# Optimization experiments

Measured on AMD Instinct MI355X. Metric: run time of the kernel, lower is better.

## Reference

```python
import jax, jax.numpy as jnp
import numpy as np

NEG_INF = -1e9  # matches masked_fill value -1000000000.0
SLOPE = 0.2     # LeakyReLU negative slope


def setup_inputs() -> dict:
    key = jax.random.key(0)
    k1, k2, k3, k4 = jax.random.split(key, 4)
    B, N, Fin, Fout = 16, 1024, 256, 256
    h = jax.random.normal(k1, (B, N, Fin), dtype=jnp.float32)
    adj = jax.random.randint(k2, (B, N, N), 0, 2, dtype=jnp.int32)
    W = jax.random.normal(k3, (Fin, Fout), dtype=jnp.float32) * (1.0 / np.sqrt(Fin))
    a = jax.random.normal(k4, (2 * Fout,), dtype=jnp.float32) * (1.0 / np.sqrt(2 * Fout))
    return {"h": h, "adj": adj, "W": W, "a": a}


def reference(h, adj, W, a):
    # h: [B,N,Fin], adj: [B,N,N] (0/1), W: [Fin,Fout], a: [2*Fout]
    Fout = W.shape[1]
    Wh = jnp.einsum("bnf,fo->bno", h, W)            # [B,N,Fout]
    a1, a2 = a[:Fout], a[Fout:]
    # e[b,i,j] = leakyrelu( Wh[b,i]·a1 + Wh[b,j]·a2 )  == a(cat(Wh_i, Wh_j))
    f1 = Wh @ a1                                     # [B,N]
    f2 = Wh @ a2                                     # [B,N]
    e = jax.nn.leaky_relu(f1[:, :, None] + f2[:, None, :], negative_slope=SLOPE)
    e = jnp.where(adj == 0, NEG_INF, e)              # mask non-edges
    attention = jax.nn.softmax(e, axis=-1)           # [B,N,N]
    # dropout is identity at eval / p=0
    h_prime = jnp.einsum("bij,bjo->bio", attention, Wh)  # [B,N,Fout]
    return h_prime
```

## Files before the change

### kernel.cpp

```cpp
#include <hip/hip_runtime.h>

typedef __attribute__((ext_vector_type(8))) short bf16x8;
typedef __attribute__((ext_vector_type(4))) float f32x4;

__device__ __forceinline__ unsigned short f2bf(float x) {
    unsigned int u = __float_as_uint(x);
    u += 0x7FFFu + ((u >> 16) & 1u);
    return (unsigned short)(u >> 16);
}

__device__ __forceinline__ void gl_lds16(const void* g, void* l) {
    __builtin_amdgcn_global_load_lds(
        (__attribute__((address_space(1))) void*)((void*)g),
        (__attribute__((address_space(3))) void*)l, 16, 0, 0);
}

__global__ __launch_bounds__(256) void prep(const float* __restrict__ W,
                                            short* __restrict__ WbT) {
    __shared__ float tile[32][33];
    const int t = threadIdx.x;
    const int bx = blockIdx.x & 7, by = blockIdx.x >> 3;
    const int r0 = by * 32, c0 = bx * 32;
    const int lr = t >> 5, lc = t & 31;
#pragma unroll
    for (int q = 0; q < 4; ++q)
        tile[q * 8 + lr][lc] = W[(r0 + q * 8 + lr) * 256 + c0 + lc];
    __syncthreads();
#pragma unroll
    for (int q = 0; q < 4; ++q)
        WbT[(c0 + q * 8 + lr) * 256 + r0 + lc] = (short)f2bf(tile[lc][q * 8 + lr]);
}

__global__ __launch_bounds__(256, 4) void wh_f12(const float* __restrict__ h,
                                                 const short* __restrict__ WbT,
                                                 const float* __restrict__ a,
                                                 short* __restrict__ WhT,
                                                 float* __restrict__ f1,
                                                 float* __restrict__ f2) {
    __shared__ short hA[16][264];
    __shared__ float sp[2][4][16];
    const int t = threadIdx.x;
    const int wid = t >> 6, lane = t & 63;
    const int quad = lane >> 4, l15 = lane & 15;
    const int m0 = blockIdx.x * 16;

    {
        const int r = t >> 4, c0 = (t & 15) * 16;
        const float* hp = h + (size_t)(m0 + r) * 256 + c0;
        float4 v0 = *(const float4*)(hp + 0), v1 = *(const float4*)(hp + 4);
        float4 v2 = *(const float4*)(hp + 8), v3 = *(const float4*)(hp + 12);
        bf16x8 w0, w1;
        w0[0] = (short)f2bf(v0.x); w0[1] = (short)f2bf(v0.y);
        w0[2] = (short)f2bf(v0.z); w0[3] = (short)f2bf(v0.w);
        w0[4] = (short)f2bf(v1.x); w0[5] = (short)f2bf(v1.y);
        w0[6] = (short)f2bf(v1.z); w0[7] = (short)f2bf(v1.w);
        w1[0] = (short)f2bf(v2.x); w1[1] = (short)f2bf(v2.y);
        w1[2] = (short)f2bf(v2.z); w1[3] = (short)f2bf(v2.w);
        w1[4] = (short)f2bf(v3.x); w1[5] = (short)f2bf(v3.y);
        w1[6] = (short)f2bf(v3.z); w1[7] = (short)f2bf(v3.w);
        *(bf16x8*)&hA[r][c0] = w0;
        *(bf16x8*)&hA[r][c0 + 8] = w1;
    }
    __syncthreads();

    f32x4 acc[4] = {};
#pragma unroll
    for (int kt = 0; kt < 8; ++kt) {
        const int k0 = kt * 32;
        bf16x8 av = *(const bf16x8*)&hA[l15][k0 + quad * 8];
#pragma unroll
        for (int ft = 0; ft < 4; ++ft) {
            const int f = wid * 64 + ft * 16 + l15;
            bf16x8 bv = *(const bf16x8*)(WbT + (size_t)f * 256 + k0 + quad * 8);
            acc[ft] = __builtin_amdgcn_mfma_f32_16x16x32_bf16(av, bv, acc[ft], 0, 0, 0);
        }
    }

    const int b = m0 >> 10;
    const int il0 = (m0 & 1023) + quad * 4;
#pragma unroll
    for (int ft = 0; ft < 4; ++ft) {
        const int f = wid * 64 + ft * 16 + l15;
        ushort4 pk;
        pk.x = f2bf(acc[ft][0]);
        pk.y = f2bf(acc[ft][1]);
        pk.z = f2bf(acc[ft][2]);
        pk.w = f2bf(acc[ft][3]);
        *(ushort4*)(WhT + ((size_t)b << 18) + (size_t)f * 1024 + il0) = pk;
    }

    float a1v[4], a2v[4];
#pragma unroll
    for (int ft = 0; ft < 4; ++ft) {
        a1v[ft] = a[wid * 64 + ft * 16 + l15];
        a2v[ft] = a[256 + wid * 64 + ft * 16 + l15];
    }
    float p1[4] = {}, p2[4] = {};
#pragma unroll
    for (int ft = 0; ft < 4; ++ft)
#pragma unroll
        for (int r = 0; r < 4; ++r) {
            p1[r] += acc[ft][r] * a1v[ft];
            p2[r] += acc[ft][r] * a2v[ft];
        }
#pragma unroll
    for (int off = 1; off < 16; off <<= 1)
#pragma unroll
        for (int r = 0; r < 4; ++r) {
            p1[r] += __shfl_xor(p1[r], off);
            p2[r] += __shfl_xor(p2[r], off);
        }
    if (l15 == 0)
#pragma unroll
        for (int r = 0; r < 4; ++r) {
            sp[0][wid][quad * 4 + r] = p1[r];
            sp[1][wid][quad * 4 + r] = p2[r];
        }
    __syncthreads();
    if (t < 16) {
        f1[m0 + t] = sp[0][0][t] + sp[0][1][t] + sp[0][2][t] + sp[0][3][t];
        f2[m0 + t] = sp[1][0][t] + sp[1][1][t] + sp[1][2][t] + sp[1][3][t];
    }
}

__global__ __launch_bounds__(256) void stats_p(const int* __restrict__ adj,
                                               const float* __restrict__ f1g,
                                               const float* __restrict__ f2g,
                                               short* __restrict__ P) {
    const int wid = threadIdx.x >> 6, lane = threadIdx.x & 63;
    const int gid = blockIdx.x * 4 + wid;
    const int b = gid >> 10;
    const int* arow = adj + (size_t)gid * 1024;
    const float* f2b = f2g + (b << 10);
    const float f1r = f1g[gid];

    float e[16];
#pragma unroll
    for (int c = 0; c < 4; ++c) {
        int4 av = *(const int4*)(arow + lane * 4 + c * 256);
        float4 fv = *(const float4*)(f2b + lane * 4 + c * 256);
        float x0 = f1r + fv.x, x1 = f1r + fv.y, x2 = f1r + fv.z, x3 = f1r + fv.w;
        e[c * 4 + 0] = av.x ? fmaxf(x0, 0.2f * x0) : -3.0e38f;
        e[c * 4 + 1] = av.y ? fmaxf(x1, 0.2f * x1) : -3.0e38f;
        e[c * 4 + 2] = av.z ? fmaxf(x2, 0.2f * x2) : -3.0e38f;
        e[c * 4 + 3] = av.w ? fmaxf(x3, 0.2f * x3) : -3.0e38f;
    }
    float m = e[0];
#pragma unroll
    for (int q = 1; q < 16; ++q) m = fmaxf(m, e[q]);
#pragma unroll
    for (int off = 32; off; off >>= 1) m = fmaxf(m, __shfl_xor(m, off));

    float p[16];
    float l = 0.f;
#pragma unroll
    for (int q = 0; q < 16; ++q) { p[q] = __expf(e[q] - m); l += p[q]; }
#pragma unroll
    for (int off = 32; off; off >>= 1) l += __shfl_xor(l, off);
    const float invl = 1.0f / l;

    short* prow = P + (size_t)gid * 1024;
#pragma unroll
    for (int c = 0; c < 4; ++c) {
        ushort4 pk;
        pk.x = f2bf(p[c * 4 + 0] * invl);
        pk.y = f2bf(p[c * 4 + 1] * invl);
        pk.z = f2bf(p[c * 4 + 2] * invl);
        pk.w = f2bf(p[c * 4 + 3] * invl);
        *(ushort4*)(prow + lane * 4 + c * 256) = pk;
    }
}

__global__ __launch_bounds__(256, 2) void agg(const short* __restrict__ P,
                                              const short* __restrict__ WhT,
                                              float* __restrict__ out) {
    __shared__ short As[128 * 32];
    __shared__ short Bs[64 * 32];

    const int t = threadIdx.x;
    const int wid = t >> 6, lane = t & 63;
    const int quad = lane >> 4, l15 = lane & 15;
    const int m0 = blockIdx.x * 128, n0 = blockIdx.y * 64, b = blockIdx.z;

    const short* Pb = P + ((size_t)b << 20);
    const short* Wb = WhT + ((size_t)b << 18);

    const int ar = t >> 2, aq = (t & 3) * 8;
    const short* ga0 = Pb + (size_t)(m0 + ar) * 1024 + aq;
    const short* ga1 = Pb + (size_t)(m0 + 64 + ar) * 1024 + aq;
    const short* gb0 = Wb + (size_t)(n0 + ar) * 1024 + aq;
    short* lA0 = As + t * 8;
    short* lA1 = As + 2048 + t * 8;
    short* lB0 = Bs + t * 8;

    f32x4 acc[2][4] = {};

    for (int k0 = 0; k0 < 1024; k0 += 32) {
        gl_lds16(ga0 + k0, lA0);
        gl_lds16(ga1 + k0, lA1);
        gl_lds16(gb0 + k0, lB0);
        __syncthreads();

        bf16x8 av[2], bv[4];
#pragma unroll
        for (int mf = 0; mf < 2; ++mf)
            av[mf] = *(const bf16x8*)(As + (wid * 32 + mf * 16 + l15) * 32 + quad * 8);
#pragma unroll
        for (int nf = 0; nf < 4; ++nf)
            bv[nf] = *(const bf16x8*)(Bs + (nf * 16 + l15) * 32 + quad * 8);
#pragma unroll
        for (int mf = 0; mf < 2; ++mf)
#pragma unroll
            for (int nf = 0; nf < 4; ++nf)
                acc[mf][nf] = __builtin_amdgcn_mfma_f32_16x16x32_bf16(av[mf], bv[nf], acc[mf][nf], 0, 0, 0);
        __syncthreads();
    }

#pragma unroll
    for (int mf = 0; mf < 2; ++mf) {
        const int i = m0 + wid * 32 + mf * 16 + quad * 4;
#pragma unroll
        for (int nf = 0; nf < 4; ++nf) {
            float* op = out + (size_t)((b << 10) + i) * 256 + n0 + nf * 16 + l15;
            op[0]   = acc[mf][nf][0];
            op[256] = acc[mf][nf][1];
            op[512] = acc[mf][nf][2];
            op[768] = acc[mf][nf][3];
        }
    }
}

extern "C" void kernel_launch(void* const* d_in, const int* in_sizes, int n_in,
                              void* d_out, int out_size, void* d_ws, size_t ws_size,
                              hipStream_t stream) {
    const float* h   = (const float*)d_in[0];
    const int*   adj = (const int*)d_in[1];
    const float* W   = (const float*)d_in[2];
    const float* a   = (const float*)d_in[3];
    float* out = (float*)d_out;

    short* WbT = (short*)d_ws;
    float* f1  = (float*)(WbT + 65536);
    float* f2  = f1 + 16384;
    short* WhT = (short*)(f2 + 16384);
    short* P   = WhT + 16 * 256 * 1024;

    prep<<<64, 256, 0, stream>>>(W, WbT);
    wh_f12<<<1024, 256, 0, stream>>>(h, WbT, a, WhT, f1, f2);
    stats_p<<<4096, 256, 0, stream>>>(adj, f1, f2, P);
    agg<<<dim3(8, 4, 16), 256, 0, stream>>>(P, WhT, out);
}
```

Measured before the change: 165.6 us.

## Retile agg GEMM with XOR-swizzled LDS and double rows per wh_f12 block

```diff
diff --git a/kernel.cpp b/kernel.cpp
--- a/kernel.cpp
+++ b/kernel.cpp
@@ -37,15 +37,16 @@
                                                  short* __restrict__ WhT,
                                                  float* __restrict__ f1,
                                                  float* __restrict__ f2) {
-    __shared__ short hA[16][264];
-    __shared__ float sp[2][4][16];
+    __shared__ short hA[32][264];
+    __shared__ float sp[2][4][32];
     const int t = threadIdx.x;
     const int wid = t >> 6, lane = t & 63;
     const int quad = lane >> 4, l15 = lane & 15;
-    const int m0 = blockIdx.x * 16;
-
-    {
-        const int r = t >> 4, c0 = (t & 15) * 16;
+    const int m0 = blockIdx.x * 32;
+
+#pragma unroll
+    for (int rr = 0; rr < 2; ++rr) {
+        const int r = rr * 16 + (t >> 4), c0 = (t & 15) * 16;
         const float* hp = h + (size_t)(m0 + r) * 256 + c0;
         float4 v0 = *(const float4*)(hp + 0), v1 = *(const float4*)(hp + 4);
         float4 v2 = *(const float4*)(hp + 8), v3 = *(const float4*)(hp + 12);
@@ -63,30 +64,37 @@
     }
     __syncthreads();
 
-    f32x4 acc[4] = {};
+    f32x4 acc[2][4] = {};
 #pragma unroll
     for (int kt = 0; kt < 8; ++kt) {
         const int k0 = kt * 32;
-        bf16x8 av = *(const bf16x8*)&hA[l15][k0 + quad * 8];
+        bf16x8 bv[4];
+#pragma unroll
+        for (int ft = 0; ft < 4; ++ft)
+            bv[ft] = *(const bf16x8*)(WbT + (size_t)(wid * 64 + ft * 16 + l15) * 256 + k0 + quad * 8);
+        bf16x8 a0 = *(const bf16x8*)&hA[l15][k0 + quad * 8];
+        bf16x8 a1 = *(const bf16x8*)&hA[16 + l15][k0 + quad * 8];
+#pragma unroll
+        for (int ft = 0; ft < 4; ++ft) {
+            acc[0][ft] = __builtin_amdgcn_mfma_f32_16x16x32_bf16(a0, bv[ft], acc[0][ft], 0, 0, 0);
+            acc[1][ft] = __builtin_amdgcn_mfma_f32_16x16x32_bf16(a1, bv[ft], acc[1][ft], 0, 0, 0);
+        }
+    }
+
+    const int b = m0 >> 10;
+#pragma unroll
+    for (int mf = 0; mf < 2; ++mf) {
+        const int il0 = (m0 & 1023) + mf * 16 + quad * 4;
 #pragma unroll
         for (int ft = 0; ft < 4; ++ft) {
             const int f = wid * 64 + ft * 16 + l15;
-            bf16x8 bv = *(const bf16x8*)(WbT + (size_t)f * 256 + k0 + quad * 8);
-            acc[ft] = __builtin_amdgcn_mfma_f32_16x16x32_bf16(av, bv, acc[ft], 0, 0, 0);
+            ushort4 pk;
+            pk.x = f2bf(acc[mf][ft][0]);
+            pk.y = f2bf(acc[mf][ft][1]);
+            pk.z = f2bf(acc[mf][ft][2]);
+            pk.w = f2bf(acc[mf][ft][3]);
+            *(ushort4*)(WhT + ((size_t)b << 18) + (size_t)f * 1024 + il0) = pk;
         }
-    }
-
-    const int b = m0 >> 10;
-    const int il0 = (m0 & 1023) + quad * 4;
-#pragma unroll
-    for (int ft = 0; ft < 4; ++ft) {
-        const int f = wid * 64 + ft * 16 + l15;
-        ushort4 pk;
-        pk.x = f2bf(acc[ft][0]);
-        pk.y = f2bf(acc[ft][1]);
-        pk.z = f2bf(acc[ft][2]);
-        pk.w = f2bf(acc[ft][3]);
-        *(ushort4*)(WhT + ((size_t)b << 18) + (size_t)f * 1024 + il0) = pk;
     }
 
     float a1v[4], a2v[4];
@@ -95,29 +103,35 @@
         a1v[ft] = a[wid * 64 + ft * 16 + l15];
         a2v[ft] = a[256 + wid * 64 + ft * 16 + l15];
     }
-    float p1[4] = {}, p2[4] = {};
-#pragma unroll
-    for (int ft = 0; ft < 4; ++ft)
-#pragma unroll
-        for (int r = 0; r < 4; ++r) {
-            p1[r] += acc[ft][r] * a1v[ft];
-            p2[r] += acc[ft][r] * a2v[ft];
-        }
+    float p1[2][4] = {}, p2[2][4] = {};
+#pragma unroll
+    for (int mf = 0; mf < 2; ++mf)
+#pragma unroll
+        for (int ft = 0; ft < 4; ++ft)
+#pragma unroll
+            for (int r = 0; r < 4; ++r) {
+                p1[mf][r] += acc[mf][ft][r] * a1v[ft];
+                p2[mf][r] += acc[mf][ft][r] * a2v[ft];
+            }
 #pragma unroll
     for (int off = 1; off < 16; off <<= 1)
 #pragma unroll
-        for (int r = 0; r < 4; ++r) {
-            p1[r] += __shfl_xor(p1[r], off);
-            p2[r] += __shfl_xor(p2[r], off);
-        }
+        for (int mf = 0; mf < 2; ++mf)
+#pragma unroll
+            for (int r = 0; r < 4; ++r) {
+                p1[mf][r] += __shfl_xor(p1[mf][r], off);
+                p2[mf][r] += __shfl_xor(p2[mf][r], off);
+            }
     if (l15 == 0)
 #pragma unroll
-        for (int r = 0; r < 4; ++r) {
-            sp[0][wid][quad * 4 + r] = p1[r];
-            sp[1][wid][quad * 4 + r] = p2[r];
-        }
+        for (int mf = 0; mf < 2; ++mf)
+#pragma unroll
+            for (int r = 0; r < 4; ++r) {
+                sp[0][wid][mf * 16 + quad * 4 + r] = p1[mf][r];
+                sp[1][wid][mf * 16 + quad * 4 + r] = p2[mf][r];
+            }
     __syncthreads();
-    if (t < 16) {
+    if (t < 32) {
         f1[m0 + t] = sp[0][0][t] + sp[0][1][t] + sp[0][2][t] + sp[0][3][t];
         f2[m0 + t] = sp[1][0][t] + sp[1][1][t] + sp[1][2][t] + sp[1][3][t];
     }
@@ -171,62 +185,63 @@
     }
 }
 
-__global__ __launch_bounds__(256, 2) void agg(const short* __restrict__ P,
+__global__ __launch_bounds__(256, 4) void agg(const short* __restrict__ P,
                                               const short* __restrict__ WhT,
                                               float* __restrict__ out) {
-    __shared__ short As[128 * 32];
-    __shared__ short Bs[64 * 32];
+    __shared__ short As[64 * 64];
+    __shared__ short Bs[64 * 64];
 
     const int t = threadIdx.x;
     const int wid = t >> 6, lane = t & 63;
     const int quad = lane >> 4, l15 = lane & 15;
-    const int m0 = blockIdx.x * 128, n0 = blockIdx.y * 64, b = blockIdx.z;
+    const int m0 = blockIdx.x * 64, n0 = blockIdx.y * 64, b = blockIdx.z;
 
     const short* Pb = P + ((size_t)b << 20);
     const short* Wb = WhT + ((size_t)b << 18);
 
-    const int ar = t >> 2, aq = (t & 3) * 8;
-    const short* ga0 = Pb + (size_t)(m0 + ar) * 1024 + aq;
-    const short* ga1 = Pb + (size_t)(m0 + 64 + ar) * 1024 + aq;
-    const short* gb0 = Wb + (size_t)(n0 + ar) * 1024 + aq;
+    const int r0 = t >> 3;
+    const int w0 = (t & 7) ^ (r0 & 7);
+    const short* gaA0 = Pb + (size_t)(m0 + r0) * 1024 + w0 * 8;
+    const short* gaA1 = Pb + (size_t)(m0 + 32 + r0) * 1024 + w0 * 8;
+    const short* gaB0 = Wb + (size_t)(n0 + r0) * 1024 + w0 * 8;
+    const short* gaB1 = Wb + (size_t)(n0 + 32 + r0) * 1024 + w0 * 8;
     short* lA0 = As + t * 8;
     short* lA1 = As + 2048 + t * 8;
     short* lB0 = Bs + t * 8;
-
-    f32x4 acc[2][4] = {};
-
-    for (int k0 = 0; k0 < 1024; k0 += 32) {
-        gl_lds16(ga0 + k0, lA0);
-        gl_lds16(ga1 + k0, lA1);
-        gl_lds16(gb0 + k0, lB0);
+    short* lB1 = Bs + 2048 + t * 8;
+
+    f32x4 acc[4] = {};
+    const int ra = wid * 16 + l15;
+
+    for (int k0 = 0; k0 < 1024; k0 += 64) {
+        gl_lds16(gaA0 + k0, lA0);
+        gl_lds16(gaA1 + k0, lA1);
+        gl_lds16(gaB0 + k0, lB0);
+        gl_lds16(gaB1 + k0, lB1);
         __syncthreads();
 
-        bf16x8 av[2], bv[4];
-#pragma unroll
-        for (int mf = 0; mf < 2; ++mf)
-            av[mf] = *(const bf16x8*)(As + (wid * 32 + mf * 16 + l15) * 32 + quad * 8);
-#pragma unroll
-        for (int nf = 0; nf < 4; ++nf)
-            bv[nf] = *(const bf16x8*)(Bs + (nf * 16 + l15) * 32 + quad * 8);
-#pragma unroll
-        for (int mf = 0; mf < 2; ++mf)
-#pragma unroll
-            for (int nf = 0; nf < 4; ++nf)
-                acc[mf][nf] = __builtin_amdgcn_mfma_f32_16x16x32_bf16(av[mf], bv[nf], acc[mf][nf], 0, 0, 0);
+#pragma unroll
+        for (int kt = 0; kt < 2; ++kt) {
+            const int w = kt * 4 + quad;
+            bf16x8 av = *(const bf16x8*)(As + ra * 64 + ((w ^ (ra & 7)) * 8));
+#pragma unroll
+            for (int nf = 0; nf < 4; ++nf) {
+                const int rb = nf * 16 + l15;
+                bf16x8 bv = *(const bf16x8*)(Bs + rb * 64 + ((w ^ (rb & 7)) * 8));
+                acc[nf] = __builtin_amdgcn_mfma_f32_16x16x32_bf16(av, bv, acc[nf], 0, 0, 0);
+            }
+        }
         __syncthreads();
     }
 
-#pragma unroll
-    for (int mf = 0; mf < 2; ++mf) {
-        const int i = m0 + wid * 32 + mf * 16 + quad * 4;
-#pragma unroll
-        for (int nf = 0; nf < 4; ++nf) {
-            float* op = out + (size_t)((b << 10) + i) * 256 + n0 + nf * 16 + l15;
-            op[0]   = acc[mf][nf][0];
-            op[256] = acc[mf][nf][1];
-            op[512] = acc[mf][nf][2];
-            op[768] = acc[mf][nf][3];
-        }
+    const int i = m0 + wid * 16 + quad * 4;
+#pragma unroll
+    for (int nf = 0; nf < 4; ++nf) {
+        float* op = out + (size_t)((b << 10) + i) * 256 + n0 + nf * 16 + l15;
+        op[0]   = acc[nf][0];
+        op[256] = acc[nf][1];
+        op[512] = acc[nf][2];
+        op[768] = acc[nf][3];
     }
 }
 
@@ -246,7 +261,7 @@
     short* P   = WhT + 16 * 256 * 1024;
 
     prep<<<64, 256, 0, stream>>>(W, WbT);
-    wh_f12<<<1024, 256, 0, stream>>>(h, WbT, a, WhT, f1, f2);
+    wh_f12<<<512, 256, 0, stream>>>(h, WbT, a, WhT, f1, f2);
     stats_p<<<4096, 256, 0, stream>>>(adj, f1, f2, P);
-    agg<<<dim3(8, 4, 16), 256, 0, stream>>>(P, WhT, out);
-}
+    agg<<<dim3(16, 4, 16), 256, 0, stream>>>(P, WhT, out);
+}
```

Result: faster. 152.2 us (-8.1%).
